# Kernel tuning notes

Hardware: AMD Instinct MI355X
Metric: run time of the kernel (lower is better)

## Reference

```python
import jax, jax.numpy as jnp
import numpy as np


def setup_inputs() -> dict:
    key = jax.random.key(0)
    kq, kk, kv = jax.random.split(key, 3)
    B, H, S, D = 4, 12, 2048, 64
    query = jax.random.normal(kq, (B, H, S, D), dtype=jnp.float32)
    k = jax.random.normal(kk, (B, H, S, D), dtype=jnp.float32)
    value = jax.random.normal(kv, (B, H, S, D), dtype=jnp.float32)
    return {"query": query, "key": k, "value": value}


def reference(query, key, value):
    # scores = Q K^T / sqrt(d_k)  -> [B, H, S, S]
    d_k = query.shape[-1]
    scale = 1.0 / jnp.sqrt(jnp.asarray(d_k, dtype=query.dtype))
    scores = jnp.einsum('bhqd,bhkd->bhqk', query, key) * scale
    attention = jax.nn.softmax(scores, axis=-1)
    # dropout p=0.0 -> identity
    output = jnp.einsum('bhqk,bhkd->bhqd', attention, value)
    return (output, attention)
```

## Files before the change

### kernel.cpp

```cpp
#include <hip/hip_runtime.h>
#include <hip/hip_bf16.h>

typedef short bf16x8_t __attribute__((ext_vector_type(8)));
typedef float f32x4_t __attribute__((ext_vector_type(4)));

#define SDIM 2048
#define DDIM 64
#define KBLK 64
#define NIT  (SDIM / KBLK)
#define NBH  48

__device__ __forceinline__ unsigned short f2bf(float f) {
    return __builtin_bit_cast(unsigned short, (__bf16)f);
}
__device__ __forceinline__ unsigned int pack2(float lo, float hi) {
    return ((unsigned int)f2bf(hi) << 16) | (unsigned int)f2bf(lo);
}
__device__ __forceinline__ bf16x8_t pack8(f32x4_t a, f32x4_t b) {
    bf16x8_t r;
    r[0] = (short)f2bf(a[0]); r[1] = (short)f2bf(a[1]);
    r[2] = (short)f2bf(a[2]); r[3] = (short)f2bf(a[3]);
    r[4] = (short)f2bf(b[0]); r[5] = (short)f2bf(b[1]);
    r[6] = (short)f2bf(b[2]); r[7] = (short)f2bf(b[3]);
    return r;
}
__device__ __forceinline__ bf16x8_t pack8s(f32x4_t a, f32x4_t b, float s) {
    bf16x8_t r;
    r[0] = (short)f2bf(a[0] * s); r[1] = (short)f2bf(a[1] * s);
    r[2] = (short)f2bf(a[2] * s); r[3] = (short)f2bf(a[3] * s);
    r[4] = (short)f2bf(b[0] * s); r[5] = (short)f2bf(b[1] * s);
    r[6] = (short)f2bf(b[2] * s); r[7] = (short)f2bf(b[3] * s);
    return r;
}
struct uint4s { unsigned int x, y, z, w; };

__device__ __forceinline__ void lds_sync() {
    asm volatile("s_waitcnt lgkmcnt(0)" ::: "memory");
    __builtin_amdgcn_s_barrier();
    asm volatile("" ::: "memory");
}

__global__ __launch_bounds__(256) void cvt_k_kernel(const float* __restrict__ K,
                                                    unsigned short* __restrict__ Kb) {
    size_t i = ((size_t)blockIdx.x * 256 + threadIdx.x) * 8;
    f32x4_t a = *(const f32x4_t*)(K + i);
    f32x4_t b = *(const f32x4_t*)(K + i + 4);
    *(bf16x8_t*)(Kb + i) = pack8(a, b);
}

__global__ __launch_bounds__(256) void tr_v_kernel(const float* __restrict__ V,
                                                   unsigned short* __restrict__ VT) {
    __shared__ unsigned short lt[64 * 72];
    const int bh = blockIdx.x >> 5;
    const int kt = blockIdx.x & 31;
    const float* Vb = V + (size_t)bh * (SDIM * DDIM) + (size_t)kt * 64 * DDIM;
    unsigned short* VTb = VT + (size_t)bh * (DDIM * SDIM) + kt * 64;
    const int t = threadIdx.x;
    {
        const int kl = t >> 2, dg = t & 3;
        const float* vp = Vb + kl * DDIM + dg * 16;
        f32x4_t v0 = *(const f32x4_t*)vp;
        f32x4_t v1 = *(const f32x4_t*)(vp + 4);
        f32x4_t v2 = *(const f32x4_t*)(vp + 8);
        f32x4_t v3 = *(const f32x4_t*)(vp + 12);
#pragma unroll
        for (int j = 0; j < 16; ++j) {
            float f = (j < 4) ? v0[j] : (j < 8) ? v1[j - 4] : (j < 12) ? v2[j - 8] : v3[j - 12];
            lt[(dg * 16 + j) * 72 + kl] = f2bf(f);
        }
    }
    __syncthreads();
    {
        const int d = t >> 2, kg = t & 3;
        bf16x8_t w0 = *(const bf16x8_t*)&lt[d * 72 + kg * 16];
        bf16x8_t w1 = *(const bf16x8_t*)&lt[d * 72 + kg * 16 + 8];
        *(bf16x8_t*)(VTb + (size_t)d * SDIM + kg * 16) = w0;
        *(bf16x8_t*)(VTb + (size_t)d * SDIM + kg * 16 + 8) = w1;
    }
}

__global__ __launch_bounds__(128, 2) void sdpa_main_kernel(
    const float* __restrict__ Q, const unsigned short* __restrict__ Kb,
    const unsigned short* __restrict__ VT, float* __restrict__ out,
    float* __restrict__ attn)
{
    __shared__ __align__(16) unsigned short Klds[KBLK * DDIM];
    __shared__ __align__(16) unsigned short Vlds[DDIM * KBLK];
    __shared__ __align__(16) float pbuf[2][16 * 64];

    const int bid = blockIdx.x;
    const int bh  = bid >> 5;
    const int qt  = bid & 31;
    const int tid = threadIdx.x;
    const int lane = tid & 63;
    const int wv   = tid >> 6;
    const int l15  = lane & 15;
    const int hi   = lane >> 4;
    const int qbase = qt * 64 + wv * 32;

    const unsigned short* KbB = Kb + (size_t)bh * (SDIM * DDIM);
    const unsigned short* VTb = VT + (size_t)bh * (DDIM * SDIM);
    float* outW  = out  + ((size_t)bh * SDIM + qbase) * DDIM;
    float* attnW = attn + (size_t)bh * SDIM * SDIM + (size_t)qbase * SDIM;
    float* pb = pbuf[wv];

    const float SC = 0.18033688011112042f;

    const float* qp0 = Q + ((size_t)bh * SDIM + qbase + l15) * DDIM + hi * 8;
    const float* qp1 = qp0 + (size_t)16 * DDIM;
    const bf16x8_t aq0_0 = pack8s(*(const f32x4_t*)qp0,        *(const f32x4_t*)(qp0 + 4), SC);
    const bf16x8_t aq1_0 = pack8s(*(const f32x4_t*)(qp0 + 32), *(const f32x4_t*)(qp0 + 36), SC);
    const bf16x8_t aq0_1 = pack8s(*(const f32x4_t*)qp1,        *(const f32x4_t*)(qp1 + 4), SC);
    const bf16x8_t aq1_1 = pack8s(*(const f32x4_t*)(qp1 + 32), *(const f32x4_t*)(qp1 + 36), SC);

    auto stage_load_K = [&](int kbase, bf16x8_t kreg[4]) {
#pragma unroll
        for (int j = 0; j < 4; ++j)
            kreg[j] = *(const bf16x8_t*)(KbB + (size_t)kbase * DDIM + (j * 128 + tid) * 8);
    };
    auto stage_write_K = [&](const bf16x8_t kreg[4]) {
#pragma unroll
        for (int j = 0; j < 4; ++j) {
            const int b = (j * 128 + tid) * 16;
            const int row = b >> 7;
            *(bf16x8_t*)((char*)Klds + (b ^ ((row & 7) << 4))) = kreg[j];
        }
    };
    auto stage_load_V = [&](int kbase, bf16x8_t vreg[4]) {
#pragma unroll
        for (int j = 0; j < 4; ++j) {
            const int row = wv * 32 + j * 8 + (lane >> 3);
            vreg[j] = *(const bf16x8_t*)(VTb + (size_t)row * SDIM + kbase + (lane & 7) * 8);
        }
    };
    auto stage_write_V = [&](const bf16x8_t vreg[4]) {
#pragma unroll
        for (int j = 0; j < 4; ++j) {
            const int row = wv * 32 + j * 8 + (lane >> 3);
            const int b = row * 128 + (lane & 7) * 16;
            *(bf16x8_t*)((char*)Vlds + (b ^ ((row & 7) << 4))) = vreg[j];
        }
    };
    auto read_kc = [&](int s, int c) -> bf16x8_t {
        const int row = s * 16 + l15;
        const int b = row * 128 + c * 64 + hi * 16;
        return *(const bf16x8_t*)((char*)Klds + (b ^ ((row & 7) << 4)));
    };
    auto read_vv = [&](int dt, int c) -> bf16x8_t {
        const int row = dt * 16 + l15;
        const int b = row * 128 + c * 64 + hi * 16;
        return *(const bf16x8_t*)((char*)Vlds + (b ^ ((row & 7) << 4)));
    };

    float rs0 = 0.f, rs1 = 0.f;
    {
        bf16x8_t kreg[4];
        stage_load_K(0, kreg);
        stage_write_K(kreg);
        lds_sync();
        for (int kb = 0; kb < NIT; ++kb) {
            bf16x8_t knx[4];
            if (kb + 1 < NIT) stage_load_K((kb + 1) * KBLK, knx);
#pragma unroll
            for (int s = 0; s < 4; ++s) {
                bf16x8_t k0 = read_kc(s, 0), k1 = read_kc(s, 1);
                f32x4_t a0 = {0.f,0.f,0.f,0.f}, a1 = {0.f,0.f,0.f,0.f};
                a0 = __builtin_amdgcn_mfma_f32_16x16x32_bf16(k0, aq0_0, a0, 0, 0, 0);
                a0 = __builtin_amdgcn_mfma_f32_16x16x32_bf16(k1, aq1_0, a0, 0, 0, 0);
                a1 = __builtin_amdgcn_mfma_f32_16x16x32_bf16(k0, aq0_1, a1, 0, 0, 0);
                a1 = __builtin_amdgcn_mfma_f32_16x16x32_bf16(k1, aq1_1, a1, 0, 0, 0);
                rs0 += __builtin_amdgcn_exp2f(a0[0]) + __builtin_amdgcn_exp2f(a0[1])
                     + __builtin_amdgcn_exp2f(a0[2]) + __builtin_amdgcn_exp2f(a0[3]);
                rs1 += __builtin_amdgcn_exp2f(a1[0]) + __builtin_amdgcn_exp2f(a1[1])
                     + __builtin_amdgcn_exp2f(a1[2]) + __builtin_amdgcn_exp2f(a1[3]);
            }
            lds_sync();
            if (kb + 1 < NIT) stage_write_K(knx);
            lds_sync();
        }
    }
    rs0 += __shfl_xor(rs0, 16); rs0 += __shfl_xor(rs0, 32);
    rs1 += __shfl_xor(rs1, 16); rs1 += __shfl_xor(rs1, 32);
    const float nlg0 = __builtin_amdgcn_logf(rs0);
    const float nlg1 = __builtin_amdgcn_logf(rs1);

    f32x4_t oacc0[4] = {{0.f,0.f,0.f,0.f},{0.f,0.f,0.f,0.f},{0.f,0.f,0.f,0.f},{0.f,0.f,0.f,0.f}};
    f32x4_t oacc1[4] = {{0.f,0.f,0.f,0.f},{0.f,0.f,0.f,0.f},{0.f,0.f,0.f,0.f},{0.f,0.f,0.f,0.f}};

    const int laneA = l15 + ((hi & 1) << 5);
    const int laneB = laneA + 16;
    const bool selHi = (hi >> 1) != 0;

    auto store_sub = [&](const f32x4_t P[4], int t, int kbase) {
#pragma unroll
        for (int g = 0; g < 4; ++g) {
            const int c4 = (g * 4 + hi) ^ ((l15 & 7) << 1);
            *(f32x4_t*)(pb + l15 * 64 + c4 * 4) = P[g];
        }
        asm volatile("s_waitcnt lgkmcnt(0)" ::: "memory");
        __builtin_amdgcn_sched_barrier(0);
#pragma unroll
        for (int j = 0; j < 4; ++j) {
            const int row = j * 4 + (lane & 3);
            const int c4 = lane >> 2;
            f32x4_t v = *(const f32x4_t*)(pb + row * 64 + (c4 ^ ((row & 7) << 1)) * 4);
            __builtin_nontemporal_store(v,
                (f32x4_t*)(attnW + (size_t)(t * 16 + row) * SDIM + kbase + c4 * 4));
        }
        asm volatile("s_waitcnt lgkmcnt(0)" ::: "memory");
        __builtin_amdgcn_sched_barrier(0);
    };
    auto build_af = [&](const f32x4_t P[4], bf16x8_t af[2]) {
        unsigned int w0[4], w1[4];
#pragma unroll
        for (int s = 0; s < 4; ++s) {
            w0[s] = pack2(P[s][0], P[s][1]);
            w1[s] = pack2(P[s][2], P[s][3]);
        }
#pragma unroll
        for (int k2 = 0; k2 < 2; ++k2) {
            const int sL = 2 * k2, sH = 2 * k2 + 1;
            unsigned int W0a = (unsigned int)__shfl((int)w0[sL], laneA);
            unsigned int W0b = (unsigned int)__shfl((int)w0[sH], laneA);
            unsigned int W1a = (unsigned int)__shfl((int)w1[sL], laneA);
            unsigned int W1b = (unsigned int)__shfl((int)w1[sH], laneA);
            unsigned int W2a = (unsigned int)__shfl((int)w0[sL], laneB);
            unsigned int W2b = (unsigned int)__shfl((int)w0[sH], laneB);
            unsigned int W3a = (unsigned int)__shfl((int)w1[sL], laneB);
            unsigned int W3b = (unsigned int)__shfl((int)w1[sH], laneB);
            uint4s W;
            W.x = selHi ? W0b : W0a;
            W.y = selHi ? W1b : W1a;
            W.z = selHi ? W2b : W2a;
            W.w = selHi ? W3b : W3a;
            af[k2] = __builtin_bit_cast(bf16x8_t, W);
        }
    };

    {
        bf16x8_t kreg[4], vreg[4];
        stage_load_K(0, kreg);
        stage_load_V(0, vreg);
        stage_write_K(kreg);
        stage_write_V(vreg);
        lds_sync();
        for (int kb = 0; kb < NIT; ++kb) {
            const int kbase = kb * KBLK;
            bf16x8_t knx[4], vnx[4];
            if (kb + 1 < NIT) {
                stage_load_K(kbase + KBLK, knx);
                stage_load_V(kbase + KBLK, vnx);
            }

            f32x4_t A0[4], A1[4];
#pragma unroll
            for (int s = 0; s < 4; ++s) {
                bf16x8_t k0 = read_kc(s, 0), k1 = read_kc(s, 1);
                f32x4_t a0 = {0.f,0.f,0.f,0.f}, a1 = {0.f,0.f,0.f,0.f};
                a0 = __builtin_amdgcn_mfma_f32_16x16x32_bf16(k0, aq0_0, a0, 0, 0, 0);
                a0 = __builtin_amdgcn_mfma_f32_16x16x32_bf16(k1, aq1_0, a0, 0, 0, 0);
                a1 = __builtin_amdgcn_mfma_f32_16x16x32_bf16(k0, aq0_1, a1, 0, 0, 0);
                a1 = __builtin_amdgcn_mfma_f32_16x16x32_bf16(k1, aq1_1, a1, 0, 0, 0);
                A0[s] = a0; A1[s] = a1;
            }

            f32x4_t P0[4], P1[4];
#pragma unroll
            for (int s = 0; s < 4; ++s) {
#pragma unroll
                for (int r = 0; r < 4; ++r) {
                    P0[s][r] = __builtin_amdgcn_exp2f(A0[s][r] - nlg0);
                    P1[s][r] = __builtin_amdgcn_exp2f(A1[s][r] - nlg1);
                }
            }

            bf16x8_t af0[2], af1[2];
            build_af(P0, af0);
            build_af(P1, af1);
#pragma unroll
            for (int dt = 0; dt < 4; ++dt) {
                bf16x8_t v0 = read_vv(dt, 0), v1 = read_vv(dt, 1);
                oacc0[dt] = __builtin_amdgcn_mfma_f32_16x16x32_bf16(af0[0], v0, oacc0[dt], 0, 0, 0);
                oacc0[dt] = __builtin_amdgcn_mfma_f32_16x16x32_bf16(af0[1], v1, oacc0[dt], 0, 0, 0);
                oacc1[dt] = __builtin_amdgcn_mfma_f32_16x16x32_bf16(af1[0], v0, oacc1[dt], 0, 0, 0);
                oacc1[dt] = __builtin_amdgcn_mfma_f32_16x16x32_bf16(af1[1], v1, oacc1[dt], 0, 0, 0);
            }

            store_sub(P0, 0, kbase);
            store_sub(P1, 1, kbase);

            lds_sync();
            if (kb + 1 < NIT) {
                stage_write_K(knx);
                stage_write_V(vnx);
            }
            lds_sync();
        }
    }

#pragma unroll
    for (int dt = 0; dt < 4; ++dt) {
#pragma unroll
        for (int r = 0; r < 4; ++r) {
            outW[(size_t)(hi * 4 + r) * DDIM + dt * 16 + l15] = oacc0[dt][r];
            outW[(size_t)(16 + hi * 4 + r) * DDIM + dt * 16 + l15] = oacc1[dt][r];
        }
    }
}

extern "C" void kernel_launch(void* const* d_in, const int* in_sizes, int n_in,
                              void* d_out, int out_size, void* d_ws, size_t ws_size,
                              hipStream_t stream) {
    const float* Q = (const float*)d_in[0];
    const float* K = (const float*)d_in[1];
    const float* V = (const float*)d_in[2];
    float* out  = (float*)d_out;
    float* attn = out + (size_t)NBH * SDIM * DDIM;

    unsigned short* Kb = (unsigned short*)d_ws;
    unsigned short* VT = Kb + (size_t)NBH * SDIM * DDIM;

    cvt_k_kernel<<<dim3((NBH * SDIM * DDIM) / (256 * 8)), dim3(256), 0, stream>>>(K, Kb);
    tr_v_kernel<<<dim3(NBH * 32), dim3(256), 0, stream>>>(V, VT);

    sdpa_main_kernel<<<dim3(NBH * 32), dim3(128), 0, stream>>>(Q, Kb, VT, out, attn);
}
```

Baseline: 251.0 us.

## Double-buffer K/V LDS tiles and widen blocks to four waves per 128 queries

The main attention kernel now uses 256-thread blocks covering 128 query rows, so each K/V tile staged into shared memory is reused by four waves instead of two. K and V tiles are double-buffered in LDS, which removes one barrier per iteration because the next tile is written into the other buffer while the current one is read. This halves the number of blocks and doubles the LDS footprint per block, which may reduce occupancy or the number of blocks resident per CU.

```diff
diff --git a/kernel.cpp b/kernel.cpp
--- a/kernel.cpp
+++ b/kernel.cpp
@@ -79,24 +79,24 @@
     }
 }
 
-__global__ __launch_bounds__(128, 2) void sdpa_main_kernel(
+__global__ __launch_bounds__(256, 2) void sdpa_main_kernel(
     const float* __restrict__ Q, const unsigned short* __restrict__ Kb,
     const unsigned short* __restrict__ VT, float* __restrict__ out,
     float* __restrict__ attn)
 {
-    __shared__ __align__(16) unsigned short Klds[KBLK * DDIM];
-    __shared__ __align__(16) unsigned short Vlds[DDIM * KBLK];
-    __shared__ __align__(16) float pbuf[2][16 * 64];
+    __shared__ __align__(16) unsigned short Klds[2][KBLK * DDIM];
+    __shared__ __align__(16) unsigned short Vlds[2][KBLK * DDIM];
+    __shared__ __align__(16) float pbuf[4][16 * 64];
 
     const int bid = blockIdx.x;
-    const int bh  = bid >> 5;
-    const int qt  = bid & 31;
+    const int bh  = bid >> 4;
+    const int qt  = bid & 15;
     const int tid = threadIdx.x;
     const int lane = tid & 63;
     const int wv   = tid >> 6;
     const int l15  = lane & 15;
     const int hi   = lane >> 4;
-    const int qbase = qt * 64 + wv * 32;
+    const int qbase = qt * 128 + wv * 32;
 
     const unsigned short* KbB = Kb + (size_t)bh * (SDIM * DDIM);
     const unsigned short* VTb = VT + (size_t)bh * (DDIM * SDIM);
@@ -113,57 +113,53 @@
     const bf16x8_t aq0_1 = pack8s(*(const f32x4_t*)qp1,        *(const f32x4_t*)(qp1 + 4), SC);
     const bf16x8_t aq1_1 = pack8s(*(const f32x4_t*)(qp1 + 32), *(const f32x4_t*)(qp1 + 36), SC);
 
-    auto stage_load_K = [&](int kbase, bf16x8_t kreg[4]) {
-#pragma unroll
-        for (int j = 0; j < 4; ++j)
-            kreg[j] = *(const bf16x8_t*)(KbB + (size_t)kbase * DDIM + (j * 128 + tid) * 8);
-    };
-    auto stage_write_K = [&](const bf16x8_t kreg[4]) {
-#pragma unroll
-        for (int j = 0; j < 4; ++j) {
-            const int b = (j * 128 + tid) * 16;
+    auto stage_load_K = [&](int kbase, bf16x8_t kreg[2]) {
+#pragma unroll
+        for (int j = 0; j < 2; ++j)
+            kreg[j] = *(const bf16x8_t*)(KbB + (size_t)kbase * DDIM + (j * 256 + tid) * 8);
+    };
+    auto stage_write_K = [&](unsigned short* dst, const bf16x8_t kreg[2]) {
+#pragma unroll
+        for (int j = 0; j < 2; ++j) {
+            const int b = (j * 256 + tid) * 16;
             const int row = b >> 7;
-            *(bf16x8_t*)((char*)Klds + (b ^ ((row & 7) << 4))) = kreg[j];
-        }
-    };
-    auto stage_load_V = [&](int kbase, bf16x8_t vreg[4]) {
-#pragma unroll
-        for (int j = 0; j < 4; ++j) {
-            const int row = wv * 32 + j * 8 + (lane >> 3);
-            vreg[j] = *(const bf16x8_t*)(VTb + (size_t)row * SDIM + kbase + (lane & 7) * 8);
-        }
-    };
-    auto stage_write_V = [&](const bf16x8_t vreg[4]) {
-#pragma unroll
-        for (int j = 0; j < 4; ++j) {
-            const int row = wv * 32 + j * 8 + (lane >> 3);
-            const int b = row * 128 + (lane & 7) * 16;
-            *(bf16x8_t*)((char*)Vlds + (b ^ ((row & 7) << 4))) = vreg[j];
-        }
-    };
-    auto read_kc = [&](int s, int c) -> bf16x8_t {
+            *(bf16x8_t*)((char*)dst + (b ^ ((row & 7) << 4))) = kreg[j];
+        }
+    };
+    auto stage_load_V = [&](int kbase, bf16x8_t vreg[2]) {
+#pragma unroll
+        for (int j = 0; j < 2; ++j) {
+            const int row = j * 32 + (tid >> 3);
+            vreg[j] = *(const bf16x8_t*)(VTb + (size_t)row * SDIM + kbase + (tid & 7) * 8);
+        }
+    };
+    auto stage_write_V = [&](unsigned short* dst, const bf16x8_t vreg[2]) {
+#pragma unroll
+        for (int j = 0; j < 2; ++j) {
+            const int row = j * 32 + (tid >> 3);
+            const int b = row * 128 + (tid & 7) * 16;
+            *(bf16x8_t*)((char*)dst + (b ^ ((row & 7) << 4))) = vreg[j];
+        }
+    };
+    auto read_tile = [&](const unsigned short* src, int s, int c) -> bf16x8_t {
         const int row = s * 16 + l15;
         const int b = row * 128 + c * 64 + hi * 16;
-        return *(const bf16x8_t*)((char*)Klds + (b ^ ((row & 7) << 4)));
-    };
-    auto read_vv = [&](int dt, int c) -> bf16x8_t {
-        const int row = dt * 16 + l15;
-        const int b = row * 128 + c * 64 + hi * 16;
-        return *(const bf16x8_t*)((char*)Vlds + (b ^ ((row & 7) << 4)));
+        return *(const bf16x8_t*)((const char*)src + (b ^ ((row & 7) << 4)));
     };
 
     float rs0 = 0.f, rs1 = 0.f;
     {
-        bf16x8_t kreg[4];
+        bf16x8_t kreg[2];
         stage_load_K(0, kreg);
-        stage_write_K(kreg);
+        stage_write_K(Klds[0], kreg);
         lds_sync();
         for (int kb = 0; kb < NIT; ++kb) {
-            bf16x8_t knx[4];
+            bf16x8_t knx[2];
             if (kb + 1 < NIT) stage_load_K((kb + 1) * KBLK, knx);
+            const unsigned short* Kc = Klds[kb & 1];
 #pragma unroll
             for (int s = 0; s < 4; ++s) {
-                bf16x8_t k0 = read_kc(s, 0), k1 = read_kc(s, 1);
+                bf16x8_t k0 = read_tile(Kc, s, 0), k1 = read_tile(Kc, s, 1);
                 f32x4_t a0 = {0.f,0.f,0.f,0.f}, a1 = {0.f,0.f,0.f,0.f};
                 a0 = __builtin_amdgcn_mfma_f32_16x16x32_bf16(k0, aq0_0, a0, 0, 0, 0);
                 a0 = __builtin_amdgcn_mfma_f32_16x16x32_bf16(k1, aq1_0, a0, 0, 0, 0);
@@ -174,8 +170,7 @@
                 rs1 += __builtin_amdgcn_exp2f(a1[0]) + __builtin_amdgcn_exp2f(a1[1])
                      + __builtin_amdgcn_exp2f(a1[2]) + __builtin_amdgcn_exp2f(a1[3]);
             }
-            lds_sync();
-            if (kb + 1 < NIT) stage_write_K(knx);
+            if (kb + 1 < NIT) stage_write_K(Klds[(kb + 1) & 1], knx);
             lds_sync();
         }
     }
@@ -238,24 +233,26 @@
     };
 
     {
-        bf16x8_t kreg[4], vreg[4];
+        bf16x8_t kreg[2], vreg[2];
         stage_load_K(0, kreg);
         stage_load_V(0, vreg);
-        stage_write_K(kreg);
-        stage_write_V(vreg);
+        stage_write_K(Klds[0], kreg);
+        stage_write_V(Vlds[0], vreg);
         lds_sync();
         for (int kb = 0; kb < NIT; ++kb) {
             const int kbase = kb * KBLK;
-            bf16x8_t knx[4], vnx[4];
+            bf16x8_t knx[2], vnx[2];
             if (kb + 1 < NIT) {
                 stage_load_K(kbase + KBLK, knx);
                 stage_load_V(kbase + KBLK, vnx);
             }
+            const unsigned short* Kc = Klds[kb & 1];
+            const unsigned short* Vc = Vlds[kb & 1];
 
             f32x4_t A0[4], A1[4];
 #pragma unroll
             for (int s = 0; s < 4; ++s) {
-                bf16x8_t k0 = read_kc(s, 0), k1 = read_kc(s, 1);
+                bf16x8_t k0 = read_tile(Kc, s, 0), k1 = read_tile(Kc, s, 1);
                 f32x4_t a0 = {0.f,0.f,0.f,0.f}, a1 = {0.f,0.f,0.f,0.f};
                 a0 = __builtin_amdgcn_mfma_f32_16x16x32_bf16(k0, aq0_0, a0, 0, 0, 0);
                 a0 = __builtin_amdgcn_mfma_f32_16x16x32_bf16(k1, aq1_0, a0, 0, 0, 0);
@@ -279,7 +276,7 @@
             build_af(P1, af1);
 #pragma unroll
             for (int dt = 0; dt < 4; ++dt) {
-                bf16x8_t v0 = read_vv(dt, 0), v1 = read_vv(dt, 1);
+                bf16x8_t v0 = read_tile(Vc, dt, 0), v1 = read_tile(Vc, dt, 1);
                 oacc0[dt] = __builtin_amdgcn_mfma_f32_16x16x32_bf16(af0[0], v0, oacc0[dt], 0, 0, 0);
                 oacc0[dt] = __builtin_amdgcn_mfma_f32_16x16x32_bf16(af0[1], v1, oacc0[dt], 0, 0, 0);
                 oacc1[dt] = __builtin_amdgcn_mfma_f32_16x16x32_bf16(af1[0], v0, oacc1[dt], 0, 0, 0);
@@ -289,10 +286,9 @@
             store_sub(P0, 0, kbase);
             store_sub(P1, 1, kbase);
 
-            lds_sync();
             if (kb + 1 < NIT) {
-                stage_write_K(knx);
-                stage_write_V(vnx);
+                stage_write_K(Klds[(kb + 1) & 1], knx);
+                stage_write_V(Vlds[(kb + 1) & 1], vnx);
             }
             lds_sync();
         }
@@ -323,5 +319,5 @@
     cvt_k_kernel<<<dim3((NBH * SDIM * DDIM) / (256 * 8)), dim3(256), 0, stream>>>(K, Kb);
     tr_v_kernel<<<dim3(NBH * 32), dim3(256), 0, stream>>>(V, VT);
 
-    sdpa_main_kernel<<<dim3(NBH * 32), dim3(128), 0, stream>>>(Q, Kb, VT, out, attn);
-}
+    sdpa_main_kernel<<<dim3(NBH * 16), dim3(256), 0, stream>>>(Q, Kb, VT, out, attn);
+}
```

New measurement: 234.2 us. -6.7%, faster.
